# Kernel optimization log

Hardware: AMD Instinct MI355X
Metric: run time of the kernel (lower is better)

The kernel has to match this reference:

```python
import jax, jax.numpy as jnp
from jax import lax
import numpy as np

WIN = 9  # default window [9, 9] in the original module


def _box_sum(x, win):
    """Sum over a win x win window, stride 1, pad win//2 (same as conv2d with ones kernel).
    Implemented separably (two 1D convs) - mathematically identical to the 2D ones-kernel conv.
    x: [B, 1, H, W] float32.
    """
    pad = win // 2
    kh = jnp.ones((1, 1, win, 1), x.dtype)
    kw = jnp.ones((1, 1, 1, win), x.dtype)
    dn = lax.conv_dimension_numbers(x.shape, kh.shape, ('NCHW', 'OIHW', 'NCHW'))
    y = lax.conv_general_dilated(x, kh, (1, 1), [(pad, pad), (0, 0)], dimension_numbers=dn)
    return lax.conv_general_dilated(y, kw, (1, 1), [(0, 0), (pad, pad)], dimension_numbers=dn)


def setup_inputs() -> dict:
    key = jax.random.key(0)
    k1, k2 = jax.random.split(key)
    shape = (32, 1, 512, 512)
    predict = jax.random.uniform(k1, shape, dtype=jnp.float32)
    target = jax.random.uniform(k2, shape, dtype=jnp.float32)
    return {"predict": predict, "target": target}


def reference(predict, target):
    win = WIN
    win_size = jnp.asarray(win * win, jnp.float32)

    I, J = predict, target
    I_sum = _box_sum(I, win)
    J_sum = _box_sum(J, win)
    I2_sum = _box_sum(I * I, win)
    J2_sum = _box_sum(J * J, win)
    IJ_sum = _box_sum(I * J, win)

    u_I = I_sum / win_size
    u_J = J_sum / win_size

    cross = IJ_sum - u_J * I_sum - u_I * J_sum + u_I * u_J * win_size
    I_var = I2_sum - 2.0 * u_I * I_sum + u_I * u_I * win_size
    J_var = J2_sum - 2.0 * u_J * J_sum + u_J * u_J * win_size

    cc = cross * cross / (I_var * J_var + 1e-6)
    return -jnp.mean(cc) + 1.0
```

## Files before the change

### kernel.cpp

```cpp
#include <hip/hip_runtime.h>


#define W 512
#define H 512
#define BH 16
#define NBANDS (H / BH)
#define NTHREADS 128

__device__ __forceinline__ float4 ld4(const float* p) {
    return *reinterpret_cast<const float4*>(p);
}

template<bool ADD>
__device__ __forceinline__ void row_accum(const float* __restrict__ Ip,
                                          const float* __restrict__ Jp,
                                          int rowbase, int x0,
                                          float vs[5][4]) {
    const float4 zz = make_float4(0.f, 0.f, 0.f, 0.f);
    float4 a0 = (x0 >= 4)     ? ld4(Ip + rowbase + x0 - 4) : zz;
    float4 a1 =                 ld4(Ip + rowbase + x0);
    float4 a2 = (x0 <= W - 8) ? ld4(Ip + rowbase + x0 + 4) : zz;
    float4 b0 = (x0 >= 4)     ? ld4(Jp + rowbase + x0 - 4) : zz;
    float4 b1 =                 ld4(Jp + rowbase + x0);
    float4 b2 = (x0 <= W - 8) ? ld4(Jp + rowbase + x0 + 4) : zz;

    float iv[12], jv[12];
    iv[0]=a0.x; iv[1]=a0.y; iv[2]=a0.z; iv[3]=a0.w;
    iv[4]=a1.x; iv[5]=a1.y; iv[6]=a1.z; iv[7]=a1.w;
    iv[8]=a2.x; iv[9]=a2.y; iv[10]=a2.z; iv[11]=a2.w;
    jv[0]=b0.x; jv[1]=b0.y; jv[2]=b0.z; jv[3]=b0.w;
    jv[4]=b1.x; jv[5]=b1.y; jv[6]=b1.z; jv[7]=b1.w;
    jv[8]=b2.x; jv[9]=b2.y; jv[10]=b2.z; jv[11]=b2.w;

    auto doq = [&](int qi, auto f) {
        float p[12];
        #pragma unroll
        for (int k = 0; k < 12; ++k) p[k] = f(k);
        float t = p[0];
        #pragma unroll
        for (int k = 1; k < 9; ++k) t += p[k];
        if (ADD) vs[qi][0] += t; else vs[qi][0] -= t;
        #pragma unroll
        for (int c = 1; c < 4; ++c) {
            t += p[c + 8] - p[c - 1];
            if (ADD) vs[qi][c] += t; else vs[qi][c] -= t;
        }
    };
    doq(0, [&](int k) { return iv[k]; });
    doq(1, [&](int k) { return jv[k]; });
    doq(2, [&](int k) { return iv[k] * iv[k]; });
    doq(3, [&](int k) { return jv[k] * jv[k]; });
    doq(4, [&](int k) { return iv[k] * jv[k]; });
}

__global__ __launch_bounds__(NTHREADS)
void ncc_main(const float* __restrict__ I, const float* __restrict__ J,
              float* __restrict__ partials) {
    const int blk  = blockIdx.x;
    const int b    = blk / NBANDS;
    const int band = blk % NBANDS;
    const int y0   = band * BH;
    const float* Ip = I + (size_t)b * (H * W);
    const float* Jp = J + (size_t)b * (H * W);
    const int x0 = (int)threadIdx.x * 4;

    float vs[5][4];
    #pragma unroll
    for (int q = 0; q < 5; ++q)
        #pragma unroll
        for (int c = 0; c < 4; ++c) vs[q][c] = 0.f;

    #pragma unroll
    for (int dr = -4; dr < 4; ++dr) {
        int r = y0 + dr;
        if (r >= 0 && r < H) row_accum<true>(Ip, Jp, r * W, x0, vs);
    }

    float cc_acc = 0.f;
    const float inv81 = 1.f / 81.f;
    for (int y = y0; y < y0 + BH; ++y) {
        int ra = y + 4;
        if (ra < H) row_accum<true>(Ip, Jp, ra * W, x0, vs);
        #pragma unroll
        for (int c = 0; c < 4; ++c) {
            float Is = vs[0][c], Js = vs[1][c];
            float I2 = vs[2][c], J2 = vs[3][c], IJ = vs[4][c];
            float cross = IJ - Is * Js * inv81;
            float Ivar  = I2 - Is * Is * inv81;
            float Jvar  = J2 - Js * Js * inv81;
            cc_acc += cross * cross / (Ivar * Jvar + 1e-6f);
        }
        int rs = y - 4;
        if (rs >= 0) row_accum<false>(Ip, Jp, rs * W, x0, vs);
    }

    #pragma unroll
    for (int off = 32; off > 0; off >>= 1)
        cc_acc += __shfl_down(cc_acc, off, 64);
    __shared__ float wsum[NTHREADS / 64];
    if ((threadIdx.x & 63) == 0) wsum[threadIdx.x >> 6] = cc_acc;
    __syncthreads();
    if (threadIdx.x == 0) partials[blockIdx.x] = wsum[0] + wsum[1];
}

__global__ __launch_bounds__(256)
void ncc_finish(const float* __restrict__ partials, float* __restrict__ out,
                int n, float inv_total) {
    float v = 0.f;
    for (int i = threadIdx.x; i < n; i += blockDim.x) v += partials[i];
    #pragma unroll
    for (int off = 32; off > 0; off >>= 1)
        v += __shfl_down(v, off, 64);
    __shared__ float wsum[4];
    if ((threadIdx.x & 63) == 0) wsum[threadIdx.x >> 6] = v;
    __syncthreads();
    if (threadIdx.x == 0) {
        float t = wsum[0] + wsum[1] + wsum[2] + wsum[3];
        out[0] = 1.0f - t * inv_total;
    }
}

extern "C" void kernel_launch(void* const* d_in, const int* in_sizes, int n_in,
                              void* d_out, int out_size, void* d_ws, size_t ws_size,
                              hipStream_t stream) {
    const float* I = (const float*)d_in[0];
    const float* J = (const float*)d_in[1];
    float* out = (float*)d_out;
    float* partials = (float*)d_ws;

    const int n = in_sizes[0];
    const int B = n / (H * W);
    const int nblocks = B * NBANDS;

    ncc_main<<<nblocks, NTHREADS, 0, stream>>>(I, J, partials);
    ncc_finish<<<1, 256, 0, stream>>>(partials, out, nblocks, 1.0f / (float)n);
}
```

Before: 119.6 us.

## Halve band height and issue add/subtract row loads together per step

Cuts the band height per block from 16 to 8 rows, doubling the block count for more parallelism. The per-row horizontal sums are restructured so the entering and leaving rows are both loaded and summed up front each iteration, which exposes more memory-level parallelism. The 9-tap horizontal sum is also reassociated into a tree to shorten the dependency chain. In exchange, each block now has a larger halo relative to its band, so more rows are reloaded in total, and register pressure rises.

```diff
diff --git a/kernel.cpp b/kernel.cpp
--- a/kernel.cpp
+++ b/kernel.cpp
@@ -3,7 +3,7 @@
 
 #define W 512
 #define H 512
-#define BH 16
+#define BH 8
 #define NBANDS (H / BH)
 #define NTHREADS 128
 
@@ -11,40 +11,46 @@
     return *reinterpret_cast<const float4*>(p);
 }
 
-template<bool ADD>
-__device__ __forceinline__ void row_accum(const float* __restrict__ Ip,
-                                          const float* __restrict__ Jp,
-                                          int rowbase, int x0,
-                                          float vs[5][4]) {
+struct Row6 { float4 a0, a1, a2, b0, b1, b2; };
+
+__device__ __forceinline__ Row6 load_row(const float* __restrict__ Ip,
+                                         const float* __restrict__ Jp,
+                                         int rowbase, int x0, bool valid) {
     const float4 zz = make_float4(0.f, 0.f, 0.f, 0.f);
-    float4 a0 = (x0 >= 4)     ? ld4(Ip + rowbase + x0 - 4) : zz;
-    float4 a1 =                 ld4(Ip + rowbase + x0);
-    float4 a2 = (x0 <= W - 8) ? ld4(Ip + rowbase + x0 + 4) : zz;
-    float4 b0 = (x0 >= 4)     ? ld4(Jp + rowbase + x0 - 4) : zz;
-    float4 b1 =                 ld4(Jp + rowbase + x0);
-    float4 b2 = (x0 <= W - 8) ? ld4(Jp + rowbase + x0 + 4) : zz;
+    Row6 r;
+    if (valid) {
+        r.a0 = (x0 >= 4)     ? ld4(Ip + rowbase + x0 - 4) : zz;
+        r.a1 =                 ld4(Ip + rowbase + x0);
+        r.a2 = (x0 <= W - 8) ? ld4(Ip + rowbase + x0 + 4) : zz;
+        r.b0 = (x0 >= 4)     ? ld4(Jp + rowbase + x0 - 4) : zz;
+        r.b1 =                 ld4(Jp + rowbase + x0);
+        r.b2 = (x0 <= W - 8) ? ld4(Jp + rowbase + x0 + 4) : zz;
+    } else {
+        r.a0 = r.a1 = r.a2 = r.b0 = r.b1 = r.b2 = zz;
+    }
+    return r;
+}
 
+__device__ __forceinline__ void hsum(const Row6& r, float h[5][4]) {
     float iv[12], jv[12];
-    iv[0]=a0.x; iv[1]=a0.y; iv[2]=a0.z; iv[3]=a0.w;
-    iv[4]=a1.x; iv[5]=a1.y; iv[6]=a1.z; iv[7]=a1.w;
-    iv[8]=a2.x; iv[9]=a2.y; iv[10]=a2.z; iv[11]=a2.w;
-    jv[0]=b0.x; jv[1]=b0.y; jv[2]=b0.z; jv[3]=b0.w;
-    jv[4]=b1.x; jv[5]=b1.y; jv[6]=b1.z; jv[7]=b1.w;
-    jv[8]=b2.x; jv[9]=b2.y; jv[10]=b2.z; jv[11]=b2.w;
+    iv[0]=r.a0.x; iv[1]=r.a0.y; iv[2]=r.a0.z; iv[3]=r.a0.w;
+    iv[4]=r.a1.x; iv[5]=r.a1.y; iv[6]=r.a1.z; iv[7]=r.a1.w;
+    iv[8]=r.a2.x; iv[9]=r.a2.y; iv[10]=r.a2.z; iv[11]=r.a2.w;
+    jv[0]=r.b0.x; jv[1]=r.b0.y; jv[2]=r.b0.z; jv[3]=r.b0.w;
+    jv[4]=r.b1.x; jv[5]=r.b1.y; jv[6]=r.b1.z; jv[7]=r.b1.w;
+    jv[8]=r.b2.x; jv[9]=r.b2.y; jv[10]=r.b2.z; jv[11]=r.b2.w;
 
     auto doq = [&](int qi, auto f) {
         float p[12];
         #pragma unroll
         for (int k = 0; k < 12; ++k) p[k] = f(k);
-        float t = p[0];
-        #pragma unroll
-        for (int k = 1; k < 9; ++k) t += p[k];
-        if (ADD) vs[qi][0] += t; else vs[qi][0] -= t;
-        #pragma unroll
-        for (int c = 1; c < 4; ++c) {
-            t += p[c + 8] - p[c - 1];
-            if (ADD) vs[qi][c] += t; else vs[qi][c] -= t;
-        }
+        float s01 = p[0] + p[1], s23 = p[2] + p[3];
+        float s45 = p[4] + p[5], s67 = p[6] + p[7];
+        float t = ((s01 + s23) + (s45 + s67)) + p[8];
+        h[qi][0] = t;
+        t += p[9]  - p[0]; h[qi][1] = t;
+        t += p[10] - p[1]; h[qi][2] = t;
+        t += p[11] - p[2]; h[qi][3] = t;
     };
     doq(0, [&](int k) { return iv[k]; });
     doq(1, [&](int k) { return jv[k]; });
@@ -73,25 +79,43 @@
     #pragma unroll
     for (int dr = -4; dr < 4; ++dr) {
         int r = y0 + dr;
-        if (r >= 0 && r < H) row_accum<true>(Ip, Jp, r * W, x0, vs);
+        if (r >= 0 && r < H) {
+            Row6 rw = load_row(Ip, Jp, r * W, x0, true);
+            float hh[5][4];
+            hsum(rw, hh);
+            #pragma unroll
+            for (int q = 0; q < 5; ++q)
+                #pragma unroll
+                for (int c = 0; c < 4; ++c) vs[q][c] += hh[q][c];
+        }
     }
 
     float cc_acc = 0.f;
     const float inv81 = 1.f / 81.f;
     for (int y = y0; y < y0 + BH; ++y) {
-        int ra = y + 4;
-        if (ra < H) row_accum<true>(Ip, Jp, ra * W, x0, vs);
+        Row6 ra = load_row(Ip, Jp, (y + 4) * W, x0, (y + 4) < H);
+        Row6 rs = load_row(Ip, Jp, (y - 4) * W, x0, (y - 4) >= 0);
+        float ha[5][4], hs[5][4];
+        hsum(ra, ha);
+        hsum(rs, hs);
+
         #pragma unroll
         for (int c = 0; c < 4; ++c) {
-            float Is = vs[0][c], Js = vs[1][c];
-            float I2 = vs[2][c], J2 = vs[3][c], IJ = vs[4][c];
+            float Is = vs[0][c] + ha[0][c];
+            float Js = vs[1][c] + ha[1][c];
+            float I2 = vs[2][c] + ha[2][c];
+            float J2 = vs[3][c] + ha[3][c];
+            float IJ = vs[4][c] + ha[4][c];
             float cross = IJ - Is * Js * inv81;
             float Ivar  = I2 - Is * Is * inv81;
             float Jvar  = J2 - Js * Js * inv81;
             cc_acc += cross * cross / (Ivar * Jvar + 1e-6f);
+            vs[0][c] = Is - hs[0][c];
+            vs[1][c] = Js - hs[1][c];
+            vs[2][c] = I2 - hs[2][c];
+            vs[3][c] = J2 - hs[3][c];
+            vs[4][c] = IJ - hs[4][c];
         }
-        int rs = y - 4;
-        if (rs >= 0) row_accum<false>(Ip, Jp, rs * W, x0, vs);
     }
 
     #pragma unroll
```

After: 118.2 us. Within noise of the previous version (-1.2%).

## Reorder box filter to vertical-first with LDS prefix-sum horizontal pass

Applied to the files above, without the earlier changes.

The kernel now keeps running vertical column sums of the five quantities and forms the horizontal 9-wide window through per-thread prefix sums exchanged with neighbour threads via double-buffered shared memory. Each thread loads one float4 per row instead of three, and the products are computed once per pixel rather than for every halo element. In exchange it adds a __syncthreads per output row. The band height drops from 16 to 8, which doubles the number of blocks but also increases redundant halo row loads. The division is replaced by a hardware reciprocal approximation, which slightly changes precision.

```diff
diff --git a/kernel.cpp b/kernel.cpp
--- a/kernel.cpp
+++ b/kernel.cpp
@@ -3,57 +3,15 @@
 
 #define W 512
 #define H 512
-#define BH 16
+#define BH 8
 #define NBANDS (H / BH)
-#define NTHREADS 128
+#define NT 128
 
 __device__ __forceinline__ float4 ld4(const float* p) {
     return *reinterpret_cast<const float4*>(p);
 }
 
-template<bool ADD>
-__device__ __forceinline__ void row_accum(const float* __restrict__ Ip,
-                                          const float* __restrict__ Jp,
-                                          int rowbase, int x0,
-                                          float vs[5][4]) {
-    const float4 zz = make_float4(0.f, 0.f, 0.f, 0.f);
-    float4 a0 = (x0 >= 4)     ? ld4(Ip + rowbase + x0 - 4) : zz;
-    float4 a1 =                 ld4(Ip + rowbase + x0);
-    float4 a2 = (x0 <= W - 8) ? ld4(Ip + rowbase + x0 + 4) : zz;
-    float4 b0 = (x0 >= 4)     ? ld4(Jp + rowbase + x0 - 4) : zz;
-    float4 b1 =                 ld4(Jp + rowbase + x0);
-    float4 b2 = (x0 <= W - 8) ? ld4(Jp + rowbase + x0 + 4) : zz;
-
-    float iv[12], jv[12];
-    iv[0]=a0.x; iv[1]=a0.y; iv[2]=a0.z; iv[3]=a0.w;
-    iv[4]=a1.x; iv[5]=a1.y; iv[6]=a1.z; iv[7]=a1.w;
-    iv[8]=a2.x; iv[9]=a2.y; iv[10]=a2.z; iv[11]=a2.w;
-    jv[0]=b0.x; jv[1]=b0.y; jv[2]=b0.z; jv[3]=b0.w;
-    jv[4]=b1.x; jv[5]=b1.y; jv[6]=b1.z; jv[7]=b1.w;
-    jv[8]=b2.x; jv[9]=b2.y; jv[10]=b2.z; jv[11]=b2.w;
-
-    auto doq = [&](int qi, auto f) {
-        float p[12];
-        #pragma unroll
-        for (int k = 0; k < 12; ++k) p[k] = f(k);
-        float t = p[0];
-        #pragma unroll
-        for (int k = 1; k < 9; ++k) t += p[k];
-        if (ADD) vs[qi][0] += t; else vs[qi][0] -= t;
-        #pragma unroll
-        for (int c = 1; c < 4; ++c) {
-            t += p[c + 8] - p[c - 1];
-            if (ADD) vs[qi][c] += t; else vs[qi][c] -= t;
-        }
-    };
-    doq(0, [&](int k) { return iv[k]; });
-    doq(1, [&](int k) { return jv[k]; });
-    doq(2, [&](int k) { return iv[k] * iv[k]; });
-    doq(3, [&](int k) { return jv[k] * jv[k]; });
-    doq(4, [&](int k) { return iv[k] * jv[k]; });
-}
-
-__global__ __launch_bounds__(NTHREADS)
+__global__ __launch_bounds__(NT)
 void ncc_main(const float* __restrict__ I, const float* __restrict__ J,
               float* __restrict__ partials) {
     const int blk  = blockIdx.x;
@@ -62,45 +20,111 @@
     const int y0   = band * BH;
     const float* Ip = I + (size_t)b * (H * W);
     const float* Jp = J + (size_t)b * (H * W);
-    const int x0 = (int)threadIdx.x * 4;
+    const int tid = threadIdx.x;
+    const int x0  = tid * 4;
 
-    float vs[5][4];
+    __shared__ float4 xch[2][5][NT + 2];
+    if (tid < 4) {
+        int p = tid & 1, s = (tid >> 1) * (NT + 1);
+        #pragma unroll
+        for (int q = 0; q < 5; ++q)
+            xch[p][q][s] = make_float4(0.f, 0.f, 0.f, 0.f);
+    }
+
+    float v[5][4];
     #pragma unroll
     for (int q = 0; q < 5; ++q)
         #pragma unroll
-        for (int c = 0; c < 4; ++c) vs[q][c] = 0.f;
+        for (int c = 0; c < 4; ++c) v[q][c] = 0.f;
+
+    auto vadd = [&](int row) {
+        float4 a = ld4(Ip + row * W + x0);
+        float4 bb = ld4(Jp + row * W + x0);
+        float av[4] = {a.x, a.y, a.z, a.w};
+        float bv[4] = {bb.x, bb.y, bb.z, bb.w};
+        #pragma unroll
+        for (int c = 0; c < 4; ++c) {
+            v[0][c] += av[c];
+            v[1][c] += bv[c];
+            v[2][c] += av[c] * av[c];
+            v[3][c] += bv[c] * bv[c];
+            v[4][c] += av[c] * bv[c];
+        }
+    };
+    auto vsub = [&](int row) {
+        float4 a = ld4(Ip + row * W + x0);
+        float4 bb = ld4(Jp + row * W + x0);
+        float av[4] = {a.x, a.y, a.z, a.w};
+        float bv[4] = {bb.x, bb.y, bb.z, bb.w};
+        #pragma unroll
+        for (int c = 0; c < 4; ++c) {
+            v[0][c] -= av[c];
+            v[1][c] -= bv[c];
+            v[2][c] -= av[c] * av[c];
+            v[3][c] -= bv[c] * bv[c];
+            v[4][c] -= av[c] * bv[c];
+        }
+    };
 
     #pragma unroll
     for (int dr = -4; dr < 4; ++dr) {
         int r = y0 + dr;
-        if (r >= 0 && r < H) row_accum<true>(Ip, Jp, r * W, x0, vs);
+        if (r >= 0) vadd(r);
     }
 
     float cc_acc = 0.f;
     const float inv81 = 1.f / 81.f;
-    for (int y = y0; y < y0 + BH; ++y) {
-        int ra = y + 4;
-        if (ra < H) row_accum<true>(Ip, Jp, ra * W, x0, vs);
+    #pragma unroll
+    for (int i = 0; i < BH; ++i) {
+        const int y = y0 + i;
+        const int p = i & 1;
+        if (y + 4 < H) vadd(y + 4);
+
+        float4 pre[5];
+        #pragma unroll
+        for (int q = 0; q < 5; ++q) {
+            float4 pr;
+            pr.x = v[q][0];
+            pr.y = pr.x + v[q][1];
+            pr.z = pr.y + v[q][2];
+            pr.w = pr.z + v[q][3];
+            pre[q] = pr;
+            xch[p][q][tid + 1] = pr;
+        }
+        __syncthreads();
+
+        float h[5][4];
+        #pragma unroll
+        for (int q = 0; q < 5; ++q) {
+            float4 L = xch[p][q][tid];
+            float4 R = xch[p][q][tid + 2];
+            float base = L.w + pre[q].w;
+            h[q][0] = base + R.x;
+            h[q][1] = (base - L.x) + R.y;
+            h[q][2] = (base - L.y) + R.z;
+            h[q][3] = (base - L.z) + R.w;
+        }
+
         #pragma unroll
         for (int c = 0; c < 4; ++c) {
-            float Is = vs[0][c], Js = vs[1][c];
-            float I2 = vs[2][c], J2 = vs[3][c], IJ = vs[4][c];
+            float Is = h[0][c], Js = h[1][c];
+            float I2 = h[2][c], J2 = h[3][c], IJ = h[4][c];
             float cross = IJ - Is * Js * inv81;
             float Ivar  = I2 - Is * Is * inv81;
             float Jvar  = J2 - Js * Js * inv81;
-            cc_acc += cross * cross / (Ivar * Jvar + 1e-6f);
+            cc_acc += cross * cross * __builtin_amdgcn_rcpf(Ivar * Jvar + 1e-6f);
         }
-        int rs = y - 4;
-        if (rs >= 0) row_accum<false>(Ip, Jp, rs * W, x0, vs);
+
+        if (y - 4 >= 0) vsub(y - 4);
     }
 
     #pragma unroll
     for (int off = 32; off > 0; off >>= 1)
         cc_acc += __shfl_down(cc_acc, off, 64);
-    __shared__ float wsum[NTHREADS / 64];
-    if ((threadIdx.x & 63) == 0) wsum[threadIdx.x >> 6] = cc_acc;
+    __shared__ float wsum[NT / 64];
+    if ((tid & 63) == 0) wsum[tid >> 6] = cc_acc;
     __syncthreads();
-    if (threadIdx.x == 0) partials[blockIdx.x] = wsum[0] + wsum[1];
+    if (tid == 0) partials[blockIdx.x] = wsum[0] + wsum[1];
 }
 
 __global__ __launch_bounds__(256)
@@ -132,6 +156,6 @@
     const int B = n / (H * W);
     const int nblocks = B * NBANDS;
 
-    ncc_main<<<nblocks, NTHREADS, 0, stream>>>(I, J, partials);
+    ncc_main<<<nblocks, NT, 0, stream>>>(I, J, partials);
     ncc_finish<<<1, 256, 0, stream>>>(partials, out, nblocks, 1.0f / (float)n);
 }
```

Result: slower. 128.4 us (+7.4%).

## Stage rows in LDS ring buffer and compute horizontal sums via wave shuffles

Applied to the files above, without the earlier changes.

The kernel is restructured so each block of 256 threads loads each input row once into an 11-row shared-memory ring, one float4 per thread split across I and J. Vertical running sums are kept per thread for 2 columns, and the 9-wide horizontal sum is built from neighbour sums via shuffles, with wave-boundary values exchanged through a small double-buffered shared edge buffer. This is meant to remove the redundant overlapping global loads and repeated horizontal sums of the old per-thread 12-wide scheme, and it replaces the divide with a hardware reciprocal. It adds a block barrier per row and fairly intricate halo logic, and the approximate reciprocal can change numerics slightly.

```diff
diff --git a/kernel.cpp b/kernel.cpp
--- a/kernel.cpp
+++ b/kernel.cpp
@@ -5,102 +5,148 @@
 #define H 512
 #define BH 16
 #define NBANDS (H / BH)
-#define NTHREADS 128
+#define NT 256
+#define RS 11
 
-__device__ __forceinline__ float4 ld4(const float* p) {
-    return *reinterpret_cast<const float4*>(p);
-}
-
-template<bool ADD>
-__device__ __forceinline__ void row_accum(const float* __restrict__ Ip,
-                                          const float* __restrict__ Jp,
-                                          int rowbase, int x0,
-                                          float vs[5][4]) {
-    const float4 zz = make_float4(0.f, 0.f, 0.f, 0.f);
-    float4 a0 = (x0 >= 4)     ? ld4(Ip + rowbase + x0 - 4) : zz;
-    float4 a1 =                 ld4(Ip + rowbase + x0);
-    float4 a2 = (x0 <= W - 8) ? ld4(Ip + rowbase + x0 + 4) : zz;
-    float4 b0 = (x0 >= 4)     ? ld4(Jp + rowbase + x0 - 4) : zz;
-    float4 b1 =                 ld4(Jp + rowbase + x0);
-    float4 b2 = (x0 <= W - 8) ? ld4(Jp + rowbase + x0 + 4) : zz;
-
-    float iv[12], jv[12];
-    iv[0]=a0.x; iv[1]=a0.y; iv[2]=a0.z; iv[3]=a0.w;
-    iv[4]=a1.x; iv[5]=a1.y; iv[6]=a1.z; iv[7]=a1.w;
-    iv[8]=a2.x; iv[9]=a2.y; iv[10]=a2.z; iv[11]=a2.w;
-    jv[0]=b0.x; jv[1]=b0.y; jv[2]=b0.z; jv[3]=b0.w;
-    jv[4]=b1.x; jv[5]=b1.y; jv[6]=b1.z; jv[7]=b1.w;
-    jv[8]=b2.x; jv[9]=b2.y; jv[10]=b2.z; jv[11]=b2.w;
-
-    auto doq = [&](int qi, auto f) {
-        float p[12];
-        #pragma unroll
-        for (int k = 0; k < 12; ++k) p[k] = f(k);
-        float t = p[0];
-        #pragma unroll
-        for (int k = 1; k < 9; ++k) t += p[k];
-        if (ADD) vs[qi][0] += t; else vs[qi][0] -= t;
-        #pragma unroll
-        for (int c = 1; c < 4; ++c) {
-            t += p[c + 8] - p[c - 1];
-            if (ADD) vs[qi][c] += t; else vs[qi][c] -= t;
-        }
-    };
-    doq(0, [&](int k) { return iv[k]; });
-    doq(1, [&](int k) { return jv[k]; });
-    doq(2, [&](int k) { return iv[k] * iv[k]; });
-    doq(3, [&](int k) { return jv[k] * jv[k]; });
-    doq(4, [&](int k) { return iv[k] * jv[k]; });
-}
-
-__global__ __launch_bounds__(NTHREADS)
+__global__ __launch_bounds__(NT)
 void ncc_main(const float* __restrict__ I, const float* __restrict__ J,
               float* __restrict__ partials) {
-    const int blk  = blockIdx.x;
-    const int b    = blk / NBANDS;
-    const int band = blk % NBANDS;
+    __shared__ float ring[RS][2][W];
+    __shared__ float edgebuf[2][6][4][5][3];
+    __shared__ float wsum[4];
+
+    const int tid  = threadIdx.x;
+    const int lane = tid & 63;
+    const int wid  = tid >> 6;
+
+    const int b    = blockIdx.x >> 5;
+    const int band = blockIdx.x & (NBANDS - 1);
     const int y0   = band * BH;
+
     const float* Ip = I + (size_t)b * (H * W);
     const float* Jp = J + (size_t)b * (H * W);
-    const int x0 = (int)threadIdx.x * 4;
 
-    float vs[5][4];
+    const int li   = tid & 127;
+    const int inp  = tid >> 7;
+    const float* src = inp ? Jp : Ip;
+    const int lcol = li * 4;
+
+    const int c0 = tid * 2;
+
+    {
+        float* ez = &edgebuf[0][0][0][0][0];
+        if (tid < 240) {
+            int p = tid / 120, r = tid % 120;
+            ez[p * 360 + (r < 60 ? r : 240 + r)] = 0.f;
+        }
+    }
+
+    float v[5][2];
     #pragma unroll
-    for (int q = 0; q < 5; ++q)
-        #pragma unroll
-        for (int c = 0; c < 4; ++c) vs[q][c] = 0.f;
+    for (int q = 0; q < 5; ++q) { v[q][0] = 0.f; v[q][1] = 0.f; }
 
-    #pragma unroll
-    for (int dr = -4; dr < 4; ++dr) {
-        int r = y0 + dr;
-        if (r >= 0 && r < H) row_accum<true>(Ip, Jp, r * W, x0, vs);
+    float4 pend = make_float4(0.f, 0.f, 0.f, 0.f);
+    {
+        int r = y0 - 4;
+        if (r >= 0) pend = *(const float4*)(src + r * W + lcol);
     }
 
     float cc_acc = 0.f;
     const float inv81 = 1.f / 81.f;
-    for (int y = y0; y < y0 + BH; ++y) {
-        int ra = y + 4;
-        if (ra < H) row_accum<true>(Ip, Jp, ra * W, x0, vs);
-        #pragma unroll
-        for (int c = 0; c < 4; ++c) {
-            float Is = vs[0][c], Js = vs[1][c];
-            float I2 = vs[2][c], J2 = vs[3][c], IJ = vs[4][c];
-            float cross = IJ - Is * Js * inv81;
-            float Ivar  = I2 - Is * Is * inv81;
-            float Jvar  = J2 - Js * Js * inv81;
-            cc_acc += cross * cross / (Ivar * Jvar + 1e-6f);
+
+    for (int t = 1; t <= 25; ++t) {
+        if (t <= 24) {
+            int ws = (t - 1) % RS;
+            *(float4*)&ring[ws][inp][lcol] = pend;
         }
-        int rs = y - 4;
-        if (rs >= 0) row_accum<false>(Ip, Jp, rs * W, x0, vs);
+        if (t <= 23) {
+            int r = y0 - 4 + t;
+            if (r >= 0 && r < H) pend = *(const float4*)(src + r * W + lcol);
+            else                 pend = make_float4(0.f, 0.f, 0.f, 0.f);
+        }
+        if (t >= 2) {
+            int as = (t - 2) % RS;
+            float2 ia = *(const float2*)&ring[as][0][c0];
+            float2 ja = *(const float2*)&ring[as][1][c0];
+            v[0][0] += ia.x;        v[0][1] += ia.y;
+            v[1][0] += ja.x;        v[1][1] += ja.y;
+            v[2][0] += ia.x * ia.x; v[2][1] += ia.y * ia.y;
+            v[3][0] += ja.x * ja.x; v[3][1] += ja.y * ja.y;
+            v[4][0] += ia.x * ja.x; v[4][1] += ia.y * ja.y;
+        }
+        if (t >= 11) {
+            int ss = t % RS;
+            float2 is = *(const float2*)&ring[ss][0][c0];
+            float2 js = *(const float2*)&ring[ss][1][c0];
+            v[0][0] -= is.x;        v[0][1] -= is.y;
+            v[1][0] -= js.x;        v[1][1] -= js.y;
+            v[2][0] -= is.x * is.x; v[2][1] -= is.y * is.y;
+            v[3][0] -= js.x * js.x; v[3][1] -= js.y * js.y;
+            v[4][0] -= is.x * js.x; v[4][1] -= is.y * js.y;
+        }
+        float S[5];
+        const int par = t & 1;
+        if (t >= 10) {
+            #pragma unroll
+            for (int q = 0; q < 5; ++q) S[q] = v[q][0] + v[q][1];
+            int cls = lane == 0 ? 0 : lane == 1 ? 1 : lane == 62 ? 2 : lane == 63 ? 3 : -1;
+            if (cls >= 0) {
+                float* e = &edgebuf[par][wid + 1][cls][0][0];
+                #pragma unroll
+                for (int q = 0; q < 5; ++q) {
+                    e[q * 3 + 0] = S[q];
+                    e[q * 3 + 1] = v[q][0];
+                    e[q * 3 + 2] = v[q][1];
+                }
+            }
+        }
+        __syncthreads();
+        if (t >= 10) {
+            const float* eL = &edgebuf[par][wid][0][0][0];
+            const float* eR = &edgebuf[par][wid + 2][0][0][0];
+            float h0[5], h1[5];
+            #pragma unroll
+            for (int q = 0; q < 5; ++q) {
+                float Sm2  = __shfl_up(S[q], 2);
+                float Sm1  = __shfl_up(S[q], 1);
+                float v0m2 = __shfl_up(v[q][0], 2);
+                float Sp1  = __shfl_down(S[q], 1);
+                float v0p2 = __shfl_down(v[q][0], 2);
+                float v1p2 = __shfl_down(v[q][1], 2);
+                if (lane == 0)       { Sm2 = eL[30 + q*3]; v0m2 = eL[30 + q*3 + 1]; Sm1 = eL[45 + q*3]; }
+                else if (lane == 1)  { Sm2 = eL[45 + q*3]; v0m2 = eL[45 + q*3 + 1]; }
+                if (lane == 63)      { Sp1 = eR[q*3]; v0p2 = eR[15 + q*3 + 1]; v1p2 = eR[15 + q*3 + 2]; }
+                else if (lane == 62) { v0p2 = eR[q*3 + 1]; v1p2 = eR[q*3 + 2]; }
+                float t9 = ((Sm2 + Sm1) + (S[q] + Sp1)) + v0p2;
+                h0[q] = t9;
+                h1[q] = (t9 - v0m2) + v1p2;
+            }
+            {
+                float Is = h0[0], Js = h0[1];
+                float u  = Is * inv81;
+                float cr = h0[4] - u * Js;
+                float Iv = h0[2] - u * Is;
+                float Jv = h0[3] - (Js * inv81) * Js;
+                cc_acc += cr * cr * __builtin_amdgcn_rcpf(Iv * Jv + 1e-6f);
+            }
+            {
+                float Is = h1[0], Js = h1[1];
+                float u  = Is * inv81;
+                float cr = h1[4] - u * Js;
+                float Iv = h1[2] - u * Is;
+                float Jv = h1[3] - (Js * inv81) * Js;
+                cc_acc += cr * cr * __builtin_amdgcn_rcpf(Iv * Jv + 1e-6f);
+            }
+        }
     }
 
     #pragma unroll
     for (int off = 32; off > 0; off >>= 1)
         cc_acc += __shfl_down(cc_acc, off, 64);
-    __shared__ float wsum[NTHREADS / 64];
-    if ((threadIdx.x & 63) == 0) wsum[threadIdx.x >> 6] = cc_acc;
+    if (lane == 0) wsum[wid] = cc_acc;
     __syncthreads();
-    if (threadIdx.x == 0) partials[blockIdx.x] = wsum[0] + wsum[1];
+    if (tid == 0)
+        partials[blockIdx.x] = (wsum[0] + wsum[1]) + (wsum[2] + wsum[3]);
 }
 
 __global__ __launch_bounds__(256)
@@ -115,7 +161,7 @@
     if ((threadIdx.x & 63) == 0) wsum[threadIdx.x >> 6] = v;
     __syncthreads();
     if (threadIdx.x == 0) {
-        float t = wsum[0] + wsum[1] + wsum[2] + wsum[3];
+        float t = (wsum[0] + wsum[1]) + (wsum[2] + wsum[3]);
         out[0] = 1.0f - t * inv_total;
     }
 }
@@ -132,6 +178,6 @@
     const int B = n / (H * W);
     const int nblocks = B * NBANDS;
 
-    ncc_main<<<nblocks, NTHREADS, 0, stream>>>(I, J, partials);
+    ncc_main<<<nblocks, NT, 0, stream>>>(I, J, partials);
     ncc_finish<<<1, 256, 0, stream>>>(partials, out, nblocks, 1.0f / (float)n);
 }
```

New measurement: 141.7 us. +18.5%, slower.
